# Kernel optimization log

Hardware: AMD Instinct MI355X
Metric: run time of the kernel (lower is better)

The kernel has to match this reference:

```python
import jax, jax.numpy as jnp
import numpy as np

N = 100000      # nodes
E = 3200000     # edges (avg degree 32)
F_IN = 16       # node_features
HID = 32        # hidden_channels
OUT = 1         # out_channels


def _glorot(key, shape, fan_in):
    return (jax.random.normal(key, shape, dtype=jnp.float32) / np.sqrt(fan_in)).astype(jnp.float32)


def setup_inputs() -> dict:
    key = jax.random.key(0)
    ks = jax.random.split(key, 18)
    inp = {
        "x": jax.random.normal(ks[0], (N, F_IN), dtype=jnp.float32),
        "edge_index": jax.random.randint(ks[1], (2, E), 0, N, dtype=jnp.int64),
        "edge_weight": jax.random.uniform(ks[2], (E,), dtype=jnp.float32),
    }
    # 6 ChebConvs (K=2): x->gate convs take F_IN, h->gate convs take HID
    names_in = [("xz", F_IN), ("hz", HID), ("xr", F_IN), ("hr", HID), ("xh", F_IN), ("hh", HID)]
    for i, (nm, fin) in enumerate(names_in):
        inp[f"W_{nm}"] = _glorot(ks[3 + i], (2, fin, HID), fin)   # [K=2, in, hidden]
        inp[f"b_{nm}"] = jnp.zeros((HID,), dtype=jnp.float32)
    inp["W_lin"] = _glorot(ks[15], (HID, OUT), HID)
    inp["b_lin"] = jnp.zeros((OUT,), dtype=jnp.float32)
    return inp


def _cheb(x, W, b, src, dst, lhat_w, n):
    # ChebConv K=2, lambda_max=2: Tx0 = x, Tx1 = L_hat @ x
    tx1 = jax.ops.segment_sum(lhat_w[:, None] * x[src], dst, num_segments=n)
    return x @ W[0] + tx1 @ W[1] + b


def reference(x, edge_index, edge_weight,
              W_xz, b_xz, W_hz, b_hz,
              W_xr, b_xr, W_hr, b_hr,
              W_xh, b_xh, W_hh, b_hh,
              W_lin, b_lin):
    n = x.shape[0]
    src, dst = edge_index[0], edge_index[1]
    # scaled Laplacian edge weights: L_hat = -D^{-1/2} A D^{-1/2} (diag cancels)
    deg = jax.ops.segment_sum(edge_weight, src, num_segments=n)
    dis = jnp.where(deg > 0, jax.lax.rsqrt(jnp.maximum(deg, 1e-12)), 0.0)
    lhat_w = -dis[src] * edge_weight * dis[dst]

    H = jnp.zeros((n, W_hz.shape[1]), dtype=x.dtype)  # initial hidden state

    Z = jax.nn.sigmoid(_cheb(x, W_xz, b_xz, src, dst, lhat_w, n)
                       + _cheb(H, W_hz, b_hz, src, dst, lhat_w, n))
    R = jax.nn.sigmoid(_cheb(x, W_xr, b_xr, src, dst, lhat_w, n)
                       + _cheb(H, W_hr, b_hr, src, dst, lhat_w, n))
    H_tilde = jnp.tanh(_cheb(x, W_xh, b_xh, src, dst, lhat_w, n)
                       + _cheb(H * R, W_hh, b_hh, src, dst, lhat_w, n))
    H_new = Z * H + (1.0 - Z) * H_tilde

    h = jax.nn.relu(H_new)
    return h @ W_lin + b_lin
```

## Files before the change

kernel.cpp:

```cpp
#include <hip/hip_runtime.h>
#include <hip/hip_fp16.h>

#define N_NODES 100000
#define N_EDGES 3200000
#define F_IN 16
#define HID 32

#define NPB 128
#define NBIN 782
#define NBLK_A 512
#define EPB (N_EDGES / NBLK_A)
#define EPB2 (EPB / 2)
#define CAPB 4608
#define CAPT 9
#define SLOTS 7

typedef unsigned long long ull;
typedef float __attribute__((ext_vector_type(4))) f4v;
typedef float __attribute__((ext_vector_type(2))) f2v;

#define OFF_GCA  0
#define OFF_GCB  784
#define OFF_DIS  1568
#define OFF_XSH  101568
#define OFF_EB   901568
#define OFF_EBS  8108480

__device__ inline float2 h2f(unsigned u)
{
    __half2 h = *reinterpret_cast<__half2*>(&u);
    return __half22float2(h);
}

__global__ __launch_bounds__(512) void scatterC(
    const int* __restrict__ src, const int* __restrict__ dst,
    const float* __restrict__ w,
    int* __restrict__ gcurA, int* __restrict__ gcurB,
    uint2* __restrict__ eb, unsigned* __restrict__ ebs)
{
    __shared__ int cnt[1024];
    __shared__ int incl[1024];
    __shared__ int curs[1024];
    __shared__ int wscr[8];
    __shared__ uint2 se[EPB];

    int t = threadIdx.x, blk = blockIdx.x;
    int base = blk * EPB;
    int lane = t & 63, wid = t >> 6;

    ull sreg[SLOTS], dreg[SLOTS], wreg[SLOTS];
#pragma unroll
    for (int i = 0; i < SLOTS; ++i) {
        int k = t + (i << 9);
        if (k < EPB2) {
            sreg[i] = __builtin_nontemporal_load((const ull*)(src + base) + k);
            dreg[i] = __builtin_nontemporal_load((const ull*)(dst + base) + k);
            wreg[i] = __builtin_nontemporal_load((const ull*)(w + base) + k);
        }
    }

    cnt[2 * t] = 0; cnt[2 * t + 1] = 0;
    __syncthreads();
#pragma unroll
    for (int i = 0; i < SLOTS; ++i) {
        int k = t + (i << 9);
        if (k < EPB2) {
            atomicAdd(&cnt[(int)((unsigned)dreg[i] >> 7)], 1);
            atomicAdd(&cnt[(int)((unsigned)(dreg[i] >> 32) >> 7)], 1);
        }
    }
    __syncthreads();
    {
        int a0 = cnt[2 * t], a1 = cnt[2 * t + 1];
        int ps = a0 + a1;
        int v = ps;
#pragma unroll
        for (int off = 1; off < 64; off <<= 1) {
            int u = __shfl_up(v, off, 64);
            if (lane >= off) v += u;
        }
        if (lane == 63) wscr[wid] = v;
        __syncthreads();
        int wpre = 0;
#pragma unroll
        for (int j = 0; j < 8; ++j) wpre += (j < wid) ? wscr[j] : 0;
        int ebase = wpre + v - ps;
        incl[2 * t]     = ebase + a0;
        incl[2 * t + 1] = ebase + ps;
        curs[2 * t]     = ebase;
        curs[2 * t + 1] = ebase + a0;
    }
    __syncthreads();
#pragma unroll
    for (int i = 0; i < SLOTS; ++i) {
        int k = t + (i << 9);
        if (k < EPB2) {
            int s0 = (int)((unsigned)sreg[i]), s1 = (int)((unsigned)(sreg[i] >> 32));
            int d0 = (int)((unsigned)dreg[i]), d1 = (int)((unsigned)(dreg[i] >> 32));
            unsigned h0 = (unsigned)__half_as_ushort(
                              __float2half_rn(__uint_as_float((unsigned)wreg[i])));
            unsigned h1 = (unsigned)__half_as_ushort(
                              __float2half_rn(__uint_as_float((unsigned)(wreg[i] >> 32))));
            int p0 = atomicAdd(&curs[d0 >> 7], 1);
            se[p0] = make_uint2((unsigned)s0 | ((unsigned)(d0 & 127) << 17),
                                ((unsigned)(d0 >> 7) << 16) | h0);
            int p1 = atomicAdd(&curs[d1 >> 7], 1);
            se[p1] = make_uint2((unsigned)s1 | ((unsigned)(d1 & 127) << 17),
                                ((unsigned)(d1 >> 7) << 16) | h1);
        }
    }
    __syncthreads();
    for (int i = t; i < NBIN; i += 512) {
        int c = cnt[i];
        curs[i] = c ? atomicAdd(&gcurA[i], c) : 0;
    }
    __syncthreads();
    for (int p = t; p < EPB; p += 512) {
        uint2 v = se[p];
        int bin = (int)(v.y >> 16);
        int local = p - (incl[bin] - cnt[bin]);
        int pos = curs[bin] + local;
        if (pos < CAPB) {
            ull pv = ((ull)(v.y & 0xFFFFu) << 32) | (ull)v.x;
            __builtin_nontemporal_store(pv, (ull*)(eb + (size_t)bin * CAPB + pos));
        }
    }
    __syncthreads();

    cnt[2 * t] = 0; cnt[2 * t + 1] = 0;
    __syncthreads();
#pragma unroll
    for (int i = 0; i < SLOTS; ++i) {
        int k = t + (i << 9);
        if (k < EPB2) {
            atomicAdd(&cnt[(int)((unsigned)sreg[i] >> 7)], 1);
            atomicAdd(&cnt[(int)((unsigned)(sreg[i] >> 32) >> 7)], 1);
        }
    }
    __syncthreads();
    {
        int a0 = cnt[2 * t], a1 = cnt[2 * t + 1];
        int ps = a0 + a1;
        int v = ps;
#pragma unroll
        for (int off = 1; off < 64; off <<= 1) {
            int u = __shfl_up(v, off, 64);
            if (lane >= off) v += u;
        }
        if (lane == 63) wscr[wid] = v;
        __syncthreads();
        int wpre = 0;
#pragma unroll
        for (int j = 0; j < 8; ++j) wpre += (j < wid) ? wscr[j] : 0;
        int ebase = wpre + v - ps;
        incl[2 * t]     = ebase + a0;
        incl[2 * t + 1] = ebase + ps;
        curs[2 * t]     = ebase;
        curs[2 * t + 1] = ebase + a0;
    }
    __syncthreads();
#pragma unroll
    for (int i = 0; i < SLOTS; ++i) {
        int k = t + (i << 9);
        if (k < EPB2) {
            int s0 = (int)((unsigned)sreg[i]), s1 = (int)((unsigned)(sreg[i] >> 32));
            unsigned h0 = (unsigned)__half_as_ushort(
                              __float2half_rn(__uint_as_float((unsigned)wreg[i])));
            unsigned h1 = (unsigned)__half_as_ushort(
                              __float2half_rn(__uint_as_float((unsigned)(wreg[i] >> 32))));
            int p0 = atomicAdd(&curs[s0 >> 7], 1);
            se[p0] = make_uint2((unsigned)s0, h0);
            int p1 = atomicAdd(&curs[s1 >> 7], 1);
            se[p1] = make_uint2((unsigned)s1, h1);
        }
    }
    __syncthreads();
    for (int i = t; i < NBIN; i += 512) {
        int c = cnt[i];
        curs[i] = c ? atomicAdd(&gcurB[i], c) : 0;
    }
    __syncthreads();
    for (int p = t; p < EPB; p += 512) {
        uint2 v = se[p];
        int bin = (int)(v.x >> 7);
        int local = p - (incl[bin] - cnt[bin]);
        int pos = curs[bin] + local;
        if (pos < CAPB) {
            unsigned rec = ((v.x & 127u) << 16) | v.y;
            __builtin_nontemporal_store(rec, ebs + (size_t)bin * CAPB + pos);
        }
    }
}

__global__ __launch_bounds__(512) void degK(
    const unsigned* __restrict__ ebs, const int* __restrict__ gcurB,
    const float* __restrict__ x, float* __restrict__ dis,
    __half* __restrict__ xsh)
{
    __shared__ float sdeg[NPB];
    int b = blockIdx.x, t = threadIdx.x;
    if (t < NPB) sdeg[t] = 0.f;
    __syncthreads();
    int m = gcurB[b];
    if (m > CAPB) m = CAPB;
    const unsigned* seg = ebs + (size_t)b * CAPB;
    for (int j = t; j < m; j += 512) {
        unsigned v = __builtin_nontemporal_load(seg + j);
        float wv = __half2float(__ushort_as_half((unsigned short)(v & 0xFFFF)));
        atomicAdd(&sdeg[v >> 16], wv);
    }
    __syncthreads();
    int n0 = b * NPB;
    if (t < NPB) {
        float dg = sdeg[t];
        float ds = (dg > 0.f) ? rsqrtf(fmaxf(dg, 1e-12f)) : 0.f;
        sdeg[t] = ds;
        if (n0 + t < N_NODES) dis[n0 + t] = ds;
    }
    __syncthreads();
    for (int i = t; i < NPB * 8; i += 512) {
        int node = n0 + (i >> 3);
        if (node < N_NODES) {
            float ds = sdeg[i >> 3];
            f2v xv = __builtin_nontemporal_load(((const f2v*)x) + node * 8 + (i & 7));
            ((__half2*)xsh)[node * 8 + (i & 7)] =
                __float22half2_rn(make_float2(xv.x * ds, xv.y * ds));
        }
    }
}

__global__ __launch_bounds__(512) void gatherNode(
    const uint2* __restrict__ eb, const int* __restrict__ gcurA,
    const float* __restrict__ dis, const __half* __restrict__ xsh,
    const float* __restrict__ x,
    const float* __restrict__ W_xz, const float* __restrict__ b_xz,
    const float* __restrict__ b_hz,
    const float* __restrict__ W_xh, const float* __restrict__ b_xh,
    const float* __restrict__ b_hh,
    const float* __restrict__ W_lin, const float* __restrict__ b_lin,
    float* __restrict__ out)
{
    __shared__ char  ovl[CAPB * 8];
    __shared__ int   cnt[NPB], scn[NPB], cur[NPB];
    __shared__ int   wtot;
    __shared__ float stx[NPB * 17];
    __shared__ float sbz[HID], sbh[HID], sWl[HID];
    __shared__ float sdis[NPB];

    uint2* se  = (uint2*)ovl;
    float* sWz = (float*)ovl;
    float* sWh = (float*)ovl + 2 * F_IN * HID;

    int t = threadIdx.x, b = blockIdx.x;
    int lane = t & 63, wid = t >> 6;
    int m = gcurA[b];
    if (m > CAPB) m = CAPB;
    const uint2* seg = eb + (size_t)b * CAPB;

    ull r[CAPT];
#pragma unroll
    for (int i = 0; i < CAPT; ++i) {
        int k = t + (i << 9);
        if (k < m) r[i] = __builtin_nontemporal_load((const ull*)(seg + k));
    }

    if (t < NPB) cnt[t] = 0;
    if (t < HID) {
        sbz[t] = b_xz[t] + b_hz[t];
        sbh[t] = b_xh[t] + b_hh[t];
        sWl[t] = W_lin[t];
    }
    if (t < NPB) {
        int n = b * NPB + t;
        sdis[t] = (n < N_NODES) ? dis[n] : 0.f;
    }
    __syncthreads();

#pragma unroll
    for (int i = 0; i < CAPT; ++i) {
        int k = t + (i << 9);
        if (k < m) atomicAdd(&cnt[(unsigned)r[i] >> 17], 1);
    }
    __syncthreads();
    {
        int v = (t < NPB) ? cnt[t] : 0;
#pragma unroll
        for (int off = 1; off < 64; off <<= 1) {
            int u = __shfl_up(v, off, 64);
            if (lane >= off) v += u;
        }
        if (t == 63) wtot = v;
        __syncthreads();
        if (t < NPB) {
            int vv = v + ((wid == 1) ? wtot : 0);
            scn[t] = vv;
            cur[t] = vv - cnt[t];
        }
    }
    __syncthreads();
#pragma unroll
    for (int i = 0; i < CAPT; ++i) {
        int k = t + (i << 9);
        if (k < m) {
            unsigned lo = (unsigned)r[i], hi = (unsigned)(r[i] >> 32);
            int p = atomicAdd(&cur[lo >> 17], 1);
            se[p] = make_uint2(lo, hi);
        }
    }
    __syncthreads();

    {
        int nloc = t >> 2;
        int h    = t & 3;
        int r1 = scn[nloc];
        int r0 = r1 - cnt[nloc];
        float dn = sdis[nloc];
        float a0 = 0.f, a1 = 0.f, a2 = 0.f, a3 = 0.f;
        int j = r0;
        for (; j + 3 < r1; j += 4) {
            uint2 e0 = se[j], e1 = se[j + 1], e2 = se[j + 2], e3 = se[j + 3];
            uint2 p0 = *(const uint2*)(xsh + ((size_t)(e0.x & 0x1FFFF) << 4) + (h << 2));
            uint2 p1 = *(const uint2*)(xsh + ((size_t)(e1.x & 0x1FFFF) << 4) + (h << 2));
            uint2 p2 = *(const uint2*)(xsh + ((size_t)(e2.x & 0x1FFFF) << 4) + (h << 2));
            uint2 p3 = *(const uint2*)(xsh + ((size_t)(e3.x & 0x1FFFF) << 4) + (h << 2));
            float lw0 = -__half2float(__ushort_as_half((unsigned short)e0.y)) * dn;
            float lw1 = -__half2float(__ushort_as_half((unsigned short)e1.y)) * dn;
            float lw2 = -__half2float(__ushort_as_half((unsigned short)e2.y)) * dn;
            float lw3 = -__half2float(__ushort_as_half((unsigned short)e3.y)) * dn;
            float2 f;
            f = h2f(p0.x); a0 = fmaf(lw0, f.x, a0); a1 = fmaf(lw0, f.y, a1);
            f = h2f(p0.y); a2 = fmaf(lw0, f.x, a2); a3 = fmaf(lw0, f.y, a3);
            f = h2f(p1.x); a0 = fmaf(lw1, f.x, a0); a1 = fmaf(lw1, f.y, a1);
            f = h2f(p1.y); a2 = fmaf(lw1, f.x, a2); a3 = fmaf(lw1, f.y, a3);
            f = h2f(p2.x); a0 = fmaf(lw2, f.x, a0); a1 = fmaf(lw2, f.y, a1);
            f = h2f(p2.y); a2 = fmaf(lw2, f.x, a2); a3 = fmaf(lw2, f.y, a3);
            f = h2f(p3.x); a0 = fmaf(lw3, f.x, a0); a1 = fmaf(lw3, f.y, a1);
            f = h2f(p3.y); a2 = fmaf(lw3, f.x, a2); a3 = fmaf(lw3, f.y, a3);
        }
        for (; j < r1; ++j) {
            uint2 e0 = se[j];
            uint2 p0 = *(const uint2*)(xsh + ((size_t)(e0.x & 0x1FFFF) << 4) + (h << 2));
            float lw0 = -__half2float(__ushort_as_half((unsigned short)e0.y)) * dn;
            float2 f;
            f = h2f(p0.x); a0 = fmaf(lw0, f.x, a0); a1 = fmaf(lw0, f.y, a1);
            f = h2f(p0.y); a2 = fmaf(lw0, f.x, a2); a3 = fmaf(lw0, f.y, a3);
        }
        float* tp = &stx[nloc * 17 + (h << 2)];
        tp[0] = a0; tp[1] = a1; tp[2] = a2; tp[3] = a3;
    }
    __syncthreads();

    for (int i = t; i < 2 * F_IN * HID; i += 512) { sWz[i] = W_xz[i]; sWh[i] = W_xh[i]; }
    __syncthreads();

    int n = b * NPB + t;
    if (t >= NPB || n >= N_NODES) return;

    float xv[F_IN], tv[F_IN];
    const f4v* xr = (const f4v*)(x + (size_t)n * F_IN);
#pragma unroll
    for (int q = 0; q < 4; ++q) {
        f4v a = __builtin_nontemporal_load(xr + q);
        xv[4 * q + 0] = a.x; xv[4 * q + 1] = a.y; xv[4 * q + 2] = a.z; xv[4 * q + 3] = a.w;
    }
#pragma unroll
    for (int k = 0; k < F_IN; ++k) tv[k] = stx[t * 17 + k];

    float acc = 0.f;
    for (int j = 0; j < HID; ++j) {
        float zp = sbz[j];
        float hp = sbh[j];
#pragma unroll
        for (int k = 0; k < F_IN; ++k) {
            zp = fmaf(xv[k], sWz[k * HID + j], zp);
            zp = fmaf(tv[k], sWz[F_IN * HID + k * HID + j], zp);
            hp = fmaf(xv[k], sWh[k * HID + j], hp);
            hp = fmaf(tv[k], sWh[F_IN * HID + k * HID + j], hp);
        }
        float z  = 1.f / (1.f + __expf(-zp));
        float ht = tanhf(hp);
        float hn = (1.f - z) * ht;
        acc = fmaf(fmaxf(hn, 0.f), sWl[j], acc);
    }
    out[n] = acc + b_lin[0];
}

extern "C" void kernel_launch(void* const* d_in, const int* in_sizes, int n_in,
                              void* d_out, int out_size, void* d_ws, size_t ws_size,
                              hipStream_t stream)
{
    const float* x     = (const float*)d_in[0];
    const int*   ei    = (const int*)d_in[1];
    const float* ew    = (const float*)d_in[2];
    const float* W_xz  = (const float*)d_in[3];
    const float* b_xz  = (const float*)d_in[4];
    const float* b_hz  = (const float*)d_in[6];
    const float* W_xh  = (const float*)d_in[11];
    const float* b_xh  = (const float*)d_in[12];
    const float* b_hh  = (const float*)d_in[14];
    const float* W_lin = (const float*)d_in[15];
    const float* b_lin = (const float*)d_in[16];
    float*       out   = (float*)d_out;

    int*      wsi = (int*)d_ws;
    float*    wsf = (float*)d_ws;

    int*      gcurA = wsi + OFF_GCA;
    int*      gcurB = wsi + OFF_GCB;
    float*    dis   = wsf + OFF_DIS;
    __half*   xsh   = (__half*)(wsi + OFF_XSH);
    uint2*    eb    = (uint2*)(wsi + OFF_EB);
    unsigned* ebs   = (unsigned*)(wsi + OFF_EBS);

    const int* src = ei;
    const int* dst = ei + N_EDGES;

    hipMemsetAsync(d_ws, 0, (size_t)OFF_DIS * 4, stream);
    scatterC<<<NBLK_A, 512, 0, stream>>>(src, dst, ew, gcurA, gcurB, eb, ebs);
    degK<<<NBIN, 512, 0, stream>>>(ebs, gcurB, x, dis, xsh);
    gatherNode<<<NBIN, 512, 0, stream>>>(eb, gcurA, dis, xsh, x,
        W_xz, b_xz, b_hz, W_xh, b_xh, b_hh, W_lin, b_lin, out);
}
```

Measured before the change: 241.3 us.

## Compute node degrees with global float atomics instead of source-binned edge scatter

```diff
diff --git a/kernel.cpp b/kernel.cpp
--- a/kernel.cpp
+++ b/kernel.cpp
@@ -24,7 +24,6 @@
 #define OFF_DIS  1568
 #define OFF_XSH  101568
 #define OFF_EB   901568
-#define OFF_EBS  8108480
 
 __device__ inline float2 h2f(unsigned u)
 {
@@ -35,8 +34,8 @@
 __global__ __launch_bounds__(512) void scatterC(
     const int* __restrict__ src, const int* __restrict__ dst,
     const float* __restrict__ w,
-    int* __restrict__ gcurA, int* __restrict__ gcurB,
-    uint2* __restrict__ eb, unsigned* __restrict__ ebs)
+    int* __restrict__ gcurA, float* __restrict__ deg,
+    uint2* __restrict__ eb)
 {
     __shared__ int cnt[1024];
     __shared__ int incl[1024];
@@ -56,6 +55,17 @@
             sreg[i] = __builtin_nontemporal_load((const ull*)(src + base) + k);
             dreg[i] = __builtin_nontemporal_load((const ull*)(dst + base) + k);
             wreg[i] = __builtin_nontemporal_load((const ull*)(w + base) + k);
+        }
+    }
+
+#pragma unroll
+    for (int i = 0; i < SLOTS; ++i) {
+        int k = t + (i << 9);
+        if (k < EPB2) {
+            float w0 = __uint_as_float((unsigned)wreg[i]);
+            float w1 = __uint_as_float((unsigned)(wreg[i] >> 32));
+            atomicAdd(deg + (int)((unsigned)sreg[i]), w0);
+            atomicAdd(deg + (int)((unsigned)(sreg[i] >> 32)), w1);
         }
     }
 
@@ -125,108 +135,31 @@
             __builtin_nontemporal_store(pv, (ull*)(eb + (size_t)bin * CAPB + pos));
         }
     }
-    __syncthreads();
-
-    cnt[2 * t] = 0; cnt[2 * t + 1] = 0;
-    __syncthreads();
-#pragma unroll
-    for (int i = 0; i < SLOTS; ++i) {
-        int k = t + (i << 9);
-        if (k < EPB2) {
-            atomicAdd(&cnt[(int)((unsigned)sreg[i] >> 7)], 1);
-            atomicAdd(&cnt[(int)((unsigned)(sreg[i] >> 32) >> 7)], 1);
-        }
-    }
-    __syncthreads();
-    {
-        int a0 = cnt[2 * t], a1 = cnt[2 * t + 1];
-        int ps = a0 + a1;
-        int v = ps;
-#pragma unroll
-        for (int off = 1; off < 64; off <<= 1) {
-            int u = __shfl_up(v, off, 64);
-            if (lane >= off) v += u;
-        }
-        if (lane == 63) wscr[wid] = v;
-        __syncthreads();
-        int wpre = 0;
-#pragma unroll
-        for (int j = 0; j < 8; ++j) wpre += (j < wid) ? wscr[j] : 0;
-        int ebase = wpre + v - ps;
-        incl[2 * t]     = ebase + a0;
-        incl[2 * t + 1] = ebase + ps;
-        curs[2 * t]     = ebase;
-        curs[2 * t + 1] = ebase + a0;
-    }
-    __syncthreads();
-#pragma unroll
-    for (int i = 0; i < SLOTS; ++i) {
-        int k = t + (i << 9);
-        if (k < EPB2) {
-            int s0 = (int)((unsigned)sreg[i]), s1 = (int)((unsigned)(sreg[i] >> 32));
-            unsigned h0 = (unsigned)__half_as_ushort(
-                              __float2half_rn(__uint_as_float((unsigned)wreg[i])));
-            unsigned h1 = (unsigned)__half_as_ushort(
-                              __float2half_rn(__uint_as_float((unsigned)(wreg[i] >> 32))));
-            int p0 = atomicAdd(&curs[s0 >> 7], 1);
-            se[p0] = make_uint2((unsigned)s0, h0);
-            int p1 = atomicAdd(&curs[s1 >> 7], 1);
-            se[p1] = make_uint2((unsigned)s1, h1);
-        }
-    }
-    __syncthreads();
-    for (int i = t; i < NBIN; i += 512) {
-        int c = cnt[i];
-        curs[i] = c ? atomicAdd(&gcurB[i], c) : 0;
-    }
-    __syncthreads();
-    for (int p = t; p < EPB; p += 512) {
-        uint2 v = se[p];
-        int bin = (int)(v.x >> 7);
-        int local = p - (incl[bin] - cnt[bin]);
-        int pos = curs[bin] + local;
-        if (pos < CAPB) {
-            unsigned rec = ((v.x & 127u) << 16) | v.y;
-            __builtin_nontemporal_store(rec, ebs + (size_t)bin * CAPB + pos);
-        }
-    }
-}
-
-__global__ __launch_bounds__(512) void degK(
-    const unsigned* __restrict__ ebs, const int* __restrict__ gcurB,
+}
+
+__global__ __launch_bounds__(256) void degK(
     const float* __restrict__ x, float* __restrict__ dis,
     __half* __restrict__ xsh)
 {
-    __shared__ float sdeg[NPB];
-    int b = blockIdx.x, t = threadIdx.x;
-    if (t < NPB) sdeg[t] = 0.f;
-    __syncthreads();
-    int m = gcurB[b];
-    if (m > CAPB) m = CAPB;
-    const unsigned* seg = ebs + (size_t)b * CAPB;
-    for (int j = t; j < m; j += 512) {
-        unsigned v = __builtin_nontemporal_load(seg + j);
-        float wv = __half2float(__ushort_as_half((unsigned short)(v & 0xFFFF)));
-        atomicAdd(&sdeg[v >> 16], wv);
-    }
-    __syncthreads();
-    int n0 = b * NPB;
-    if (t < NPB) {
-        float dg = sdeg[t];
-        float ds = (dg > 0.f) ? rsqrtf(fmaxf(dg, 1e-12f)) : 0.f;
-        sdeg[t] = ds;
-        if (n0 + t < N_NODES) dis[n0 + t] = ds;
-    }
-    __syncthreads();
-    for (int i = t; i < NPB * 8; i += 512) {
-        int node = n0 + (i >> 3);
-        if (node < N_NODES) {
-            float ds = sdeg[i >> 3];
-            f2v xv = __builtin_nontemporal_load(((const f2v*)x) + node * 8 + (i & 7));
-            ((__half2*)xsh)[node * 8 + (i & 7)] =
-                __float22half2_rn(make_float2(xv.x * ds, xv.y * ds));
-        }
-    }
+    int n = blockIdx.x * 256 + threadIdx.x;
+    if (n >= N_NODES) return;
+    float dg = dis[n];
+    float ds = (dg > 0.f) ? rsqrtf(fmaxf(dg, 1e-12f)) : 0.f;
+    dis[n] = ds;
+
+    const f4v* xr = (const f4v*)(x + (size_t)n * F_IN);
+    unsigned hw[8];
+#pragma unroll
+    for (int q = 0; q < 4; ++q) {
+        f4v a = __builtin_nontemporal_load(xr + q);
+        __half2 h0 = __float22half2_rn(make_float2(a.x * ds, a.y * ds));
+        __half2 h1 = __float22half2_rn(make_float2(a.z * ds, a.w * ds));
+        hw[2 * q]     = *reinterpret_cast<unsigned*>(&h0);
+        hw[2 * q + 1] = *reinterpret_cast<unsigned*>(&h1);
+    }
+    uint4* op = (uint4*)(xsh + (size_t)n * F_IN);
+    op[0] = make_uint4(hw[0], hw[1], hw[2], hw[3]);
+    op[1] = make_uint4(hw[4], hw[5], hw[6], hw[7]);
 }
 
 __global__ __launch_bounds__(512) void gatherNode(
@@ -406,18 +339,16 @@
     float*    wsf = (float*)d_ws;
 
     int*      gcurA = wsi + OFF_GCA;
-    int*      gcurB = wsi + OFF_GCB;
     float*    dis   = wsf + OFF_DIS;
     __half*   xsh   = (__half*)(wsi + OFF_XSH);
     uint2*    eb    = (uint2*)(wsi + OFF_EB);
-    unsigned* ebs   = (unsigned*)(wsi + OFF_EBS);
 
     const int* src = ei;
     const int* dst = ei + N_EDGES;
 
-    hipMemsetAsync(d_ws, 0, (size_t)OFF_DIS * 4, stream);
-    scatterC<<<NBLK_A, 512, 0, stream>>>(src, dst, ew, gcurA, gcurB, eb, ebs);
-    degK<<<NBIN, 512, 0, stream>>>(ebs, gcurB, x, dis, xsh);
+    hipMemsetAsync(d_ws, 0, (size_t)(OFF_DIS + N_NODES) * 4, stream);
+    scatterC<<<NBLK_A, 512, 0, stream>>>(src, dst, ew, gcurA, dis, eb);
+    degK<<<(N_NODES + 255) / 256, 256, 0, stream>>>(x, dis, xsh);
     gatherNode<<<NBIN, 512, 0, stream>>>(eb, gcurA, dis, xsh, x,
         W_xz, b_xz, b_hz, W_xh, b_xh, b_hh, W_lin, b_lin, out);
 }
```

New measurement: 339.4 us. +40.7%, slower.
